# Performance work log

Measured on AMD Instinct MI355X. Metric: run time of the kernel, lower is better.

## Reference

```python
import jax, jax.numpy as jnp
import numpy as np

B, DIM, EMBDIM = 32, 512, 512
MEMSIZE, MEMSEQ = 32, 64
VOCAB = 50257


def setup_inputs() -> dict:
    key = jax.random.key(0)
    ks = jax.random.split(key, 10)
    inp = {
        'enc': jax.random.normal(ks[0], (B, DIM), jnp.float32),
        'encsumm': jax.random.normal(ks[1], (B, DIM), jnp.float32),
        'embsumm': jax.random.normal(ks[2], (B, EMBDIM), jnp.float32),
        'memencs': jax.random.normal(ks[3], (B, MEMSIZE, MEMSEQ, DIM), jnp.float32),
        'memencsumm': jax.random.normal(ks[4], (B, MEMSIZE, MEMSEQ, DIM), jnp.float32),
        'memembsumm': jax.random.normal(ks[5], (B, MEMSIZE, MEMSEQ, EMBDIM), jnp.float32),
        'memmask': jnp.ones((B, MEMSIZE, MEMSEQ), jnp.float32),
        'memids': jax.random.randint(ks[6], (B, MEMSIZE, MEMSEQ), 0, VOCAB, jnp.int64 if jax.config.jax_enable_x64 else jnp.int32),
        'W_out': jax.random.normal(ks[7], (VOCAB, 2 * DIM), jnp.float32) * 0.02,
        'b_out': jnp.zeros((VOCAB,), jnp.float32),
        'W_mix': jax.random.normal(ks[8], (2, 2 * DIM), jnp.float32) * 0.02,
        'b_mix': jnp.zeros((2,), jnp.float32),
        'unktok_mask': jnp.ones((VOCAB,), jnp.float32),  # no unktoks
    }
    return inp


def reference(enc, encsumm, embsumm, memencs, memencsumm, memembsumm, memmask,
              memids, W_out, b_out, W_mix, b_mix, unktok_mask):
    # copy branch: attention over flattened memory, scatter-add into vocab
    query = jnp.concatenate([embsumm, jnp.zeros_like(encsumm), enc], axis=-1)        # (B, 2*dim+embdim)
    keys = jnp.concatenate([memembsumm, jnp.zeros_like(memencsumm), memencs], axis=-1)  # (B, M, Z, 2*dim+embdim)
    w = jnp.einsum('bd,bmzd->bmz', query, keys) + jnp.log(memmask)
    b = w.shape[0]
    w = w.reshape(b, -1)                                    # (B, M*Z)
    alphas = jax.nn.softmax(w, axis=-1)
    mem_flat = memencs.reshape(b, -1, memencs.shape[-1])    # (B, M*Z, dim)
    mem_enc_summ = jnp.einsum('bm,bmd->bd', alphas, mem_flat)
    toks = memids.reshape(b, -1)                            # (B, M*Z)
    rows = jnp.arange(b)[:, None]
    vocsize = W_out.shape[0]
    probs_mem = jnp.zeros((b, vocsize), alphas.dtype).at[rows, toks].add(alphas)
    # generation branch
    h = jnp.concatenate([encsumm, enc], axis=-1)            # (B, 2*dim)
    logits_gen = h @ W_out.T + b_out + jnp.log(unktok_mask)[None, :]
    probs_gen = jax.nn.softmax(logits_gen, axis=-1)
    # mixer combine
    mix = jax.nn.softmax(h @ W_mix.T + b_mix, axis=-1)      # (B, 2)
    probs = mix[:, 0:1] * probs_gen + mix[:, 1:2] * probs_mem
    # original stack/gather trick: selects probs where nonzero, zeros where zero -> identity
    probs = jnp.where(probs != 0, probs, jnp.zeros_like(probs))
    return probs, mem_enc_summ
```

## Files before the change

kernel.cpp:

```cpp
#include <hip/hip_runtime.h>
#include <hip/hip_bf16.h>

#define NB   32
#define DIMK 512
#define MM   32
#define ZZ   64
#define MZV  2048
#define VOC  50257
#define NK4  1571

typedef __attribute__((ext_vector_type(8))) short  short8;
typedef __attribute__((ext_vector_type(4))) float  f32x4;
typedef __attribute__((ext_vector_type(8))) unsigned short ushort8;

#define WS_W      0
#define WS_PVEC   (WS_W + NB*MZV)
#define WS_LSTAT  (WS_PVEC + NB*MM*DIMK)
#define WS_GSTATW (WS_LSTAT + NB*MM*2)
#define WS_MIX    (WS_GSTATW + NB*2)
#define WS_GPART  (WS_MIX + NB*2)
#define WS_H      (WS_GPART + NB*32*2)

__device__ __forceinline__ ushort8 cvt8(float4 a, float4 b) {
    union { ushort8 u; __hip_bfloat162 h[4]; } r;
    r.h[0] = __float22bfloat162_rn(make_float2(a.x, a.y));
    r.h[1] = __float22bfloat162_rn(make_float2(a.z, a.w));
    r.h[2] = __float22bfloat162_rn(make_float2(b.x, b.y));
    r.h[3] = __float22bfloat162_rn(make_float2(b.z, b.w));
    return r.u;
}

typedef const __attribute__((address_space(1))) void* gas_t;
typedef __attribute__((address_space(3))) void*       las_t;
__device__ __forceinline__ void gload16(const void* g, void* l) {
    __builtin_amdgcn_global_load_lds((gas_t)g, (las_t)l, 16, 0, 0);
}

__global__ void k0_stageh(const float* __restrict__ encsumm, const float* __restrict__ enc,
                          float* __restrict__ ws)
{
    int b = blockIdx.x;
    int c = threadIdx.x * 4;
    const float* src = (c < DIMK) ? (encsumm + b*DIMK + c) : (enc + b*DIMK + (c - DIMK));
    float4 v = *(const float4*)src;
    union { ushort4 u; __hip_bfloat162 h[2]; } o;
    o.h[0] = __float22bfloat162_rn(make_float2(v.x, v.y));
    o.h[1] = __float22bfloat162_rn(make_float2(v.z, v.w));
    *(ushort4*)((unsigned short*)(ws + WS_H) + b*1024 + c) = o.u;
}

__global__ __launch_bounds__(256, 4) void k14_fused(
    const float* __restrict__ enc, const float* __restrict__ embsumm,
    const float* __restrict__ memencs, const float* __restrict__ memembsumm,
    const float* __restrict__ memmask,
    const unsigned short* __restrict__ hbf,
    const float* __restrict__ W_out, const float* __restrict__ b_out,
    const float* __restrict__ unk, float* __restrict__ out,
    float* __restrict__ ws)
{
    __shared__ __align__(16) union {
        struct { float sacc[4][DIMK]; float sst[4][2]; } s1;
        struct { float w[2][2048]; unsigned short a[2][2048]; } s4;
    } smem;

    int bid = blockIdx.x;
    int tid = threadIdx.x, wid = tid >> 6, lane = tid & 63;
    bool isK1; int sub;
    if (bid < 2048) { isK1 = ((bid & 1) == 0); sub = bid >> 1; }
    else            { isK1 = false;            sub = bid - 1024; }

    if (isK1) {
        int b = sub >> 5, m = sub & 31;
        int c0 = lane * 4, c1 = c0 + 256;
        const float* encb = enc + b * DIMK;
        const float* embb = embsumm + b * DIMK;
        float4 qe0 = *(const float4*)(encb + c0);
        float4 qe1 = *(const float4*)(encb + c1);
        float4 qm0 = *(const float4*)(embb + c0);
        float4 qm1 = *(const float4*)(embb + c1);
        const float* meb = memencs    + (long)(b*MM + m) * ZZ * DIMK;
        const float* mmb = memembsumm + (long)(b*MM + m) * ZZ * DIMK;
        const float* mkb = memmask    + (long)(b*MM + m) * ZZ;
        float* w_ws = ws + WS_W + b*MZV + m*ZZ;

        float lmax = -3.0e38f, lsum = 0.f;
        float4 a0 = make_float4(0.f,0.f,0.f,0.f), a1 = make_float4(0.f,0.f,0.f,0.f);

        for (int z = wid; z < ZZ; z += 4) {
            const float* mer = meb + z*DIMK;
            const float* mmr = mmb + z*DIMK;
            float4 e0 = *(const float4*)(mer + c0);
            float4 e1 = *(const float4*)(mer + c1);
            float4 s0 = *(const float4*)(mmr + c0);
            float4 s1 = *(const float4*)(mmr + c1);
            float d = e0.x*qe0.x + e0.y*qe0.y + e0.z*qe0.z + e0.w*qe0.w
                    + e1.x*qe1.x + e1.y*qe1.y + e1.z*qe1.z + e1.w*qe1.w
                    + s0.x*qm0.x + s0.y*qm0.y + s0.z*qm0.z + s0.w*qm0.w
                    + s1.x*qm1.x + s1.y*qm1.y + s1.z*qm1.z + s1.w*qm1.w;
            #pragma unroll
            for (int off = 32; off; off >>= 1) d += __shfl_xor(d, off);
            d += logf(mkb[z]);
            if (lane == 0) w_ws[z] = d;
            float nm = fmaxf(lmax, d);
            float sc = __expf(lmax - nm);
            float e  = __expf(d - nm);
            lsum = lsum * sc + e;
            a0.x = a0.x*sc + e*e0.x; a0.y = a0.y*sc + e*e0.y;
            a0.z = a0.z*sc + e*e0.z; a0.w = a0.w*sc + e*e0.w;
            a1.x = a1.x*sc + e*e1.x; a1.y = a1.y*sc + e*e1.y;
            a1.z = a1.z*sc + e*e1.z; a1.w = a1.w*sc + e*e1.w;
            lmax = nm;
        }

        *(float4*)&smem.s1.sacc[wid][c0] = a0;
        *(float4*)&smem.s1.sacc[wid][c1] = a1;
        if (lane == 0) { smem.s1.sst[wid][0] = lmax; smem.s1.sst[wid][1] = lsum; }
        __syncthreads();
        float bm = fmaxf(fmaxf(smem.s1.sst[0][0], smem.s1.sst[1][0]),
                         fmaxf(smem.s1.sst[2][0], smem.s1.sst[3][0]));
        float sc0 = __expf(smem.s1.sst[0][0]-bm), sc1 = __expf(smem.s1.sst[1][0]-bm);
        float sc2 = __expf(smem.s1.sst[2][0]-bm), sc3 = __expf(smem.s1.sst[3][0]-bm);
        float bs = smem.s1.sst[0][1]*sc0 + smem.s1.sst[1][1]*sc1
                 + smem.s1.sst[2][1]*sc2 + smem.s1.sst[3][1]*sc3;
        int d0 = tid * 2;
        float2 v0 = *(float2*)&smem.s1.sacc[0][d0];
        float2 v1 = *(float2*)&smem.s1.sacc[1][d0];
        float2 v2 = *(float2*)&smem.s1.sacc[2][d0];
        float2 v3 = *(float2*)&smem.s1.sacc[3][d0];
        float p0 = v0.x*sc0 + v1.x*sc1 + v2.x*sc2 + v3.x*sc3;
        float p1 = v0.y*sc0 + v1.y*sc1 + v2.y*sc2 + v3.y*sc3;
        float* pv = ws + WS_PVEC + (long)(b*MM+m)*DIMK + d0;
        pv[0] = p0; pv[1] = p1;
        if (tid == 0) { float* ls = ws + WS_LSTAT + (b*MM+m)*2; ls[0] = bm; ls[1] = bs; }
    } else {
        int wv = wid >> 1, wb = wid & 1;
        int vt = sub * 32;

        int idx0 = (wid*2 + 0)*64 + lane;
        int idx1 = (wid*2 + 1)*64 + lane;
        int wr0 = idx0 >> 4, wq0 = idx0 & 15;
        int wr1 = idx1 >> 4, wq1 = idx1 & 15;
        const float* wsrc0 = W_out + (long)min(vt + wr0, VOC-1)*1024 + ((wq0 ^ (wr0 & 7))*4);
        const float* wsrc1 = W_out + (long)min(vt + wr1, VOC-1)*1024 + ((wq1 ^ (wr1 & 7))*4);
        int aidx = wid*64 + lane;
        int ar = aidx >> 3, ag = aidx & 7;
        const unsigned short* asrc = hbf + ar*1024 + ((ag ^ (ar & 7))*8);

#define ISSUE(c, buf) do {                                            \
            gload16(wsrc0 + (c)*64, &smem.s4.w[buf][idx0*4]);         \
            gload16(wsrc1 + (c)*64, &smem.s4.w[buf][idx1*4]);         \
            gload16(asrc  + (c)*64, &smem.s4.a[buf][aidx*8]); } while (0)

        int lg = lane >> 4, ln = lane & 15;
        int vrow = wv*16 + ln;
        int ab   = wb*16 + ln;
        f32x4 acc = {0.f, 0.f, 0.f, 0.f};

        ISSUE(0, 0);
        ISSUE(1, 1);
        __syncthreads();

        for (int c = 0; c < 16; ++c) {
            int buf = c & 1;
            #pragma unroll
            for (int s = 0; s < 2; ++s) {
                int q = s*8 + lg*2;
                float4 b0 = *(const float4*)&smem.s4.w[buf][vrow*64 + ((q    ) ^ (vrow & 7))*4];
                float4 b1 = *(const float4*)&smem.s4.w[buf][vrow*64 + ((q + 1) ^ (vrow & 7))*4];
                int g = s*4 + lg;
                short8 afrag = *(const short8*)&smem.s4.a[buf][ab*64 + ((g ^ (ab & 7)))*8];
                ushort8 bu = cvt8(b0, b1);
                short8 bfrag = *(short8*)&bu;
                acc = __builtin_amdgcn_mfma_f32_16x16x32_bf16(afrag, bfrag, acc, 0, 0, 0);
            }
            __syncthreads();
            if (c + 2 < 16) ISSUE(c + 2, buf);
        }
#undef ISSUE

        int v = vt + vrow;
        if (v < VOC) {
            float bias = b_out[v] + logf(unk[v]);
            #pragma unroll
            for (int rr = 0; rr < 4; ++rr) {
                int m = wb*16 + lg*4 + rr;
                out[(long)m*VOC + v] = acc[rr] + bias;
            }
        }
    }
}

__global__ __launch_bounds__(256) void k2_comb(
    const float* __restrict__ encsumm, const float* __restrict__ enc,
    const float* __restrict__ W_mix, const float* __restrict__ b_mix,
    float* __restrict__ out, float* __restrict__ ws)
{
    int b = blockIdx.x, tid = threadIdx.x;
    const float* ls = ws + WS_LSTAT + b*MM*2;
    float gm = -3.0e38f;
    #pragma unroll
    for (int m = 0; m < MM; m++) gm = fmaxf(gm, ls[m*2]);
    float gs = 0.f;
    #pragma unroll
    for (int m = 0; m < MM; m++) gs += ls[m*2+1] * __expf(ls[m*2] - gm);
    if (tid == 0) { ws[WS_GSTATW + b*2] = gm; ws[WS_GSTATW + b*2 + 1] = gs; }
    float inv = 1.0f / gs;
    int d0 = tid * 2;
    float p0 = 0.f, p1 = 0.f;
    for (int m = 0; m < MM; m++) {
        float sc = __expf(ls[m*2] - gm);
        const float* pv = ws + WS_PVEC + (long)(b*MM+m)*DIMK + d0;
        p0 += pv[0]*sc; p1 += pv[1]*sc;
    }
    out[(long)NB*VOC + b*DIMK + d0]     = p0 * inv;
    out[(long)NB*VOC + b*DIMK + d0 + 1] = p1 * inv;

    if (tid < 64) {
        int l = tid;
        float m0 = 0.f, m1 = 0.f;
        #pragma unroll
        for (int p = 0; p < 4; p++) {
            int cc = l*4 + p*256;
            float4 h4 = (cc < 512) ? *(const float4*)(encsumm + b*DIMK + cc)
                                   : *(const float4*)(enc + b*DIMK + cc - 512);
            float4 w0 = *(const float4*)(W_mix + cc);
            float4 w1 = *(const float4*)(W_mix + 1024 + cc);
            m0 += h4.x*w0.x + h4.y*w0.y + h4.z*w0.z + h4.w*w0.w;
            m1 += h4.x*w1.x + h4.y*w1.y + h4.z*w1.z + h4.w*w1.w;
        }
        #pragma unroll
        for (int off = 32; off; off >>= 1) { m0 += __shfl_xor(m0, off); m1 += __shfl_xor(m1, off); }
        if (l == 0) {
            m0 += b_mix[0]; m1 += b_mix[1];
            float mx = fmaxf(m0, m1);
            float e0 = __expf(m0-mx), e1 = __expf(m1-mx);
            float s = e0 + e1;
            ws[WS_MIX + b*2] = e0/s; ws[WS_MIX + b*2 + 1] = e1/s;
        }
    }
}

__global__ __launch_bounds__(256) void k5_gstat(const float* __restrict__ logits, float* __restrict__ ws)
{
    int chunk = blockIdx.x, b = blockIdx.y, tid = threadIdx.x;
    const int CH = (VOC + 31) / 32;
    int v0 = chunk * CH;
    int v1 = min(VOC, v0 + CH);
    float m = -3.0e38f, s = 0.f;
    for (int v = v0 + tid; v < v1; v += 256) {
        float x = logits[(long)b*VOC + v];
        float nm = fmaxf(m, x);
        s = s*__expf(m - nm) + __expf(x - nm);
        m = nm;
    }
    #pragma unroll
    for (int off = 32; off; off >>= 1) {
        float om = __shfl_xor(m, off), os = __shfl_xor(s, off);
        float nm = fmaxf(m, om);
        s = s*__expf(m - nm) + os*__expf(om - nm);
        m = nm;
    }
    __shared__ float sm[4], ssum[4];
    int wid = tid >> 6, lane = tid & 63;
    if (lane == 0) { sm[wid] = m; ssum[wid] = s; }
    __syncthreads();
    if (tid == 0) {
        float gm = fmaxf(fmaxf(sm[0], sm[1]), fmaxf(sm[2], sm[3]));
        float gs = ssum[0]*__expf(sm[0]-gm) + ssum[1]*__expf(sm[1]-gm)
                 + ssum[2]*__expf(sm[2]-gm) + ssum[3]*__expf(sm[3]-gm);
        ws[WS_GPART + (b*32 + chunk)*2]     = gm;
        ws[WS_GPART + (b*32 + chunk)*2 + 1] = gs;
    }
}

__global__ __launch_bounds__(256) void k6_final(float* __restrict__ probs, const float* __restrict__ ws)
{
    int v = blockIdx.x*256 + threadIdx.x;
    int b = blockIdx.y;
    float gm = -3.0e38f;
    #pragma unroll
    for (int i = 0; i < 32; ++i) gm = fmaxf(gm, ws[WS_GPART + (b*32+i)*2]);
    float gs = 0.f;
    #pragma unroll
    for (int i = 0; i < 32; ++i)
        gs += ws[WS_GPART + (b*32+i)*2 + 1] * __expf(ws[WS_GPART + (b*32+i)*2] - gm);
    if (v >= VOC) return;
    float mix0 = ws[WS_MIX + b*2];
    long idx = (long)b*VOC + v;
    probs[idx] = mix0 * __expf(probs[idx] - gm) / gs;
}

__global__ __launch_bounds__(256) void k7_scatter(const int* __restrict__ memids,
                                                  const float* __restrict__ ws,
                                                  float* __restrict__ probs)
{
    int idx = blockIdx.x*256 + threadIdx.x;
    int b = idx >> 11, mz = idx & 2047;
    float gm = ws[WS_GSTATW + b*2], gs = ws[WS_GSTATW + b*2 + 1];
    float mix1 = ws[WS_MIX + b*2 + 1];
    float alpha = __expf(ws[WS_W + b*MZV + mz] - gm) / gs;
    int tok = memids[b*MZV + mz];
    atomicAdd(&probs[(long)b*VOC + tok], mix1 * alpha);
}

extern "C" void kernel_launch(void* const* d_in, const int* in_sizes, int n_in,
                              void* d_out, int out_size, void* d_ws, size_t ws_size,
                              hipStream_t stream)
{
    const float* enc        = (const float*)d_in[0];
    const float* encsumm    = (const float*)d_in[1];
    const float* embsumm    = (const float*)d_in[2];
    const float* memencs    = (const float*)d_in[3];
    const float* memembsumm = (const float*)d_in[5];
    const float* memmask    = (const float*)d_in[6];
    const int*   memids     = (const int*)d_in[7];
    const float* W_out      = (const float*)d_in[8];
    const float* b_out      = (const float*)d_in[9];
    const float* W_mix      = (const float*)d_in[10];
    const float* b_mix      = (const float*)d_in[11];
    const float* unk        = (const float*)d_in[12];
    float* out = (float*)d_out;
    float* ws  = (float*)d_ws;

    hipLaunchKernelGGL(k0_stageh, dim3(NB), dim3(256), 0, stream, encsumm, enc, ws);
    hipLaunchKernelGGL(k14_fused, dim3(1024 + NK4), dim3(256), 0, stream,
                       enc, embsumm, memencs, memembsumm, memmask,
                       (const unsigned short*)(ws + WS_H), W_out, b_out, unk, out, ws);
    hipLaunchKernelGGL(k2_comb, dim3(NB), dim3(256), 0, stream,
                       encsumm, enc, W_mix, b_mix, out, ws);
    hipLaunchKernelGGL(k5_gstat, dim3(32, NB), dim3(256), 0, stream, out, ws);
    hipLaunchKernelGGL(k6_final, dim3((VOC + 255)/256, NB), dim3(256), 0, stream, out, ws);
    hipLaunchKernelGGL(k7_scatter, dim3(NB*MZV/256), dim3(256), 0, stream, memids, ws, out);
}
```

Baseline: 137.1 us.

## Fold h bf16 staging into GEMM loop and merge comb/gstat kernels

Result: faster. 129.4 us (-5.7%).

```diff
diff --git a/kernel.cpp b/kernel.cpp
--- a/kernel.cpp
+++ b/kernel.cpp
@@ -19,7 +19,6 @@
 #define WS_GSTATW (WS_LSTAT + NB*MM*2)
 #define WS_MIX    (WS_GSTATW + NB*2)
 #define WS_GPART  (WS_MIX + NB*2)
-#define WS_H      (WS_GPART + NB*32*2)
 
 __device__ __forceinline__ ushort8 cvt8(float4 a, float4 b) {
     union { ushort8 u; __hip_bfloat162 h[4]; } r;
@@ -36,24 +35,11 @@
     __builtin_amdgcn_global_load_lds((gas_t)g, (las_t)l, 16, 0, 0);
 }
 
-__global__ void k0_stageh(const float* __restrict__ encsumm, const float* __restrict__ enc,
-                          float* __restrict__ ws)
-{
-    int b = blockIdx.x;
-    int c = threadIdx.x * 4;
-    const float* src = (c < DIMK) ? (encsumm + b*DIMK + c) : (enc + b*DIMK + (c - DIMK));
-    float4 v = *(const float4*)src;
-    union { ushort4 u; __hip_bfloat162 h[2]; } o;
-    o.h[0] = __float22bfloat162_rn(make_float2(v.x, v.y));
-    o.h[1] = __float22bfloat162_rn(make_float2(v.z, v.w));
-    *(ushort4*)((unsigned short*)(ws + WS_H) + b*1024 + c) = o.u;
-}
-
-__global__ __launch_bounds__(256, 4) void k14_fused(
+__global__ __launch_bounds__(256, 6) void k14_fused(
     const float* __restrict__ enc, const float* __restrict__ embsumm,
+    const float* __restrict__ encsumm,
     const float* __restrict__ memencs, const float* __restrict__ memembsumm,
     const float* __restrict__ memmask,
-    const unsigned short* __restrict__ hbf,
     const float* __restrict__ W_out, const float* __restrict__ b_out,
     const float* __restrict__ unk, float* __restrict__ out,
     float* __restrict__ ws)
@@ -142,22 +128,29 @@
         int wr1 = idx1 >> 4, wq1 = idx1 & 15;
         const float* wsrc0 = W_out + (long)min(vt + wr0, VOC-1)*1024 + ((wq0 ^ (wr0 & 7))*4);
         const float* wsrc1 = W_out + (long)min(vt + wr1, VOC-1)*1024 + ((wq1 ^ (wr1 & 7))*4);
-        int aidx = wid*64 + lane;
-        int ar = aidx >> 3, ag = aidx & 7;
-        const unsigned short* asrc = hbf + ar*1024 + ((ag ^ (ar & 7))*8);
-
-#define ISSUE(c, buf) do {                                            \
+        int ar = tid >> 3, ag = tid & 7;
+        const float* hs0 = encsumm + ar*DIMK + ag*8;
+        const float* hs1 = enc     + ar*DIMK + ag*8;
+        int awpos = ar*64 + ((ag ^ (ar & 7))*8);
+
+#define ISSUE_W(c, buf) do {                                          \
             gload16(wsrc0 + (c)*64, &smem.s4.w[buf][idx0*4]);         \
-            gload16(wsrc1 + (c)*64, &smem.s4.w[buf][idx1*4]);         \
-            gload16(asrc  + (c)*64, &smem.s4.a[buf][aidx*8]); } while (0)
+            gload16(wsrc1 + (c)*64, &smem.s4.w[buf][idx1*4]); } while (0)
+#define LOADA(c) do { const float* hp = ((c) < 8 ? hs0 + (c)*64 : hs1 + ((c)-8)*64); \
+            af0 = *(const float4*)(hp); af1 = *(const float4*)(hp + 4); } while (0)
+#define WRITEA(buf) do { *(ushort8*)&smem.s4.a[buf][awpos] = cvt8(af0, af1); } while (0)
 
         int lg = lane >> 4, ln = lane & 15;
         int vrow = wv*16 + ln;
         int ab   = wb*16 + ln;
         f32x4 acc = {0.f, 0.f, 0.f, 0.f};
-
-        ISSUE(0, 0);
-        ISSUE(1, 1);
+        float4 af0, af1;
+
+        LOADA(0); WRITEA(0);
+        LOADA(1); WRITEA(1);
+        LOADA(2);
+        ISSUE_W(0, 0);
+        ISSUE_W(1, 1);
         __syncthreads();
 
         for (int c = 0; c < 16; ++c) {
@@ -174,9 +167,15 @@
                 acc = __builtin_amdgcn_mfma_f32_16x16x32_bf16(afrag, bfrag, acc, 0, 0, 0);
             }
             __syncthreads();
-            if (c + 2 < 16) ISSUE(c + 2, buf);
-        }
-#undef ISSUE
+            if (c + 2 < 16) {
+                WRITEA(buf);
+                ISSUE_W(c + 2, buf);
+                if (c + 3 < 16) LOADA(c + 3);
+            }
+        }
+#undef ISSUE_W
+#undef LOADA
+#undef WRITEA
 
         int v = vt + vrow;
         if (v < VOC) {
@@ -190,86 +189,88 @@
     }
 }
 
-__global__ __launch_bounds__(256) void k2_comb(
+__global__ __launch_bounds__(256) void k2k5(
     const float* __restrict__ encsumm, const float* __restrict__ enc,
     const float* __restrict__ W_mix, const float* __restrict__ b_mix,
     float* __restrict__ out, float* __restrict__ ws)
 {
-    int b = blockIdx.x, tid = threadIdx.x;
-    const float* ls = ws + WS_LSTAT + b*MM*2;
-    float gm = -3.0e38f;
-    #pragma unroll
-    for (int m = 0; m < MM; m++) gm = fmaxf(gm, ls[m*2]);
-    float gs = 0.f;
-    #pragma unroll
-    for (int m = 0; m < MM; m++) gs += ls[m*2+1] * __expf(ls[m*2] - gm);
-    if (tid == 0) { ws[WS_GSTATW + b*2] = gm; ws[WS_GSTATW + b*2 + 1] = gs; }
-    float inv = 1.0f / gs;
-    int d0 = tid * 2;
-    float p0 = 0.f, p1 = 0.f;
-    for (int m = 0; m < MM; m++) {
-        float sc = __expf(ls[m*2] - gm);
-        const float* pv = ws + WS_PVEC + (long)(b*MM+m)*DIMK + d0;
-        p0 += pv[0]*sc; p1 += pv[1]*sc;
-    }
-    out[(long)NB*VOC + b*DIMK + d0]     = p0 * inv;
-    out[(long)NB*VOC + b*DIMK + d0 + 1] = p1 * inv;
-
-    if (tid < 64) {
-        int l = tid;
-        float m0 = 0.f, m1 = 0.f;
+    int bid = blockIdx.x, tid = threadIdx.x;
+    if (bid < 32) {
+        int b = bid;
+        const float* ls = ws + WS_LSTAT + b*MM*2;
+        float gm = -3.0e38f;
         #pragma unroll
-        for (int p = 0; p < 4; p++) {
-            int cc = l*4 + p*256;
-            float4 h4 = (cc < 512) ? *(const float4*)(encsumm + b*DIMK + cc)
-                                   : *(const float4*)(enc + b*DIMK + cc - 512);
-            float4 w0 = *(const float4*)(W_mix + cc);
-            float4 w1 = *(const float4*)(W_mix + 1024 + cc);
-            m0 += h4.x*w0.x + h4.y*w0.y + h4.z*w0.z + h4.w*w0.w;
-            m1 += h4.x*w1.x + h4.y*w1.y + h4.z*w1.z + h4.w*w1.w;
-        }
+        for (int m = 0; m < MM; m++) gm = fmaxf(gm, ls[m*2]);
+        float gs = 0.f;
         #pragma unroll
-        for (int off = 32; off; off >>= 1) { m0 += __shfl_xor(m0, off); m1 += __shfl_xor(m1, off); }
-        if (l == 0) {
-            m0 += b_mix[0]; m1 += b_mix[1];
-            float mx = fmaxf(m0, m1);
-            float e0 = __expf(m0-mx), e1 = __expf(m1-mx);
-            float s = e0 + e1;
-            ws[WS_MIX + b*2] = e0/s; ws[WS_MIX + b*2 + 1] = e1/s;
-        }
-    }
-}
-
-__global__ __launch_bounds__(256) void k5_gstat(const float* __restrict__ logits, float* __restrict__ ws)
-{
-    int chunk = blockIdx.x, b = blockIdx.y, tid = threadIdx.x;
-    const int CH = (VOC + 31) / 32;
-    int v0 = chunk * CH;
-    int v1 = min(VOC, v0 + CH);
-    float m = -3.0e38f, s = 0.f;
-    for (int v = v0 + tid; v < v1; v += 256) {
-        float x = logits[(long)b*VOC + v];
-        float nm = fmaxf(m, x);
-        s = s*__expf(m - nm) + __expf(x - nm);
-        m = nm;
-    }
-    #pragma unroll
-    for (int off = 32; off; off >>= 1) {
-        float om = __shfl_xor(m, off), os = __shfl_xor(s, off);
-        float nm = fmaxf(m, om);
-        s = s*__expf(m - nm) + os*__expf(om - nm);
-        m = nm;
-    }
-    __shared__ float sm[4], ssum[4];
-    int wid = tid >> 6, lane = tid & 63;
-    if (lane == 0) { sm[wid] = m; ssum[wid] = s; }
-    __syncthreads();
-    if (tid == 0) {
-        float gm = fmaxf(fmaxf(sm[0], sm[1]), fmaxf(sm[2], sm[3]));
-        float gs = ssum[0]*__expf(sm[0]-gm) + ssum[1]*__expf(sm[1]-gm)
-                 + ssum[2]*__expf(sm[2]-gm) + ssum[3]*__expf(sm[3]-gm);
-        ws[WS_GPART + (b*32 + chunk)*2]     = gm;
-        ws[WS_GPART + (b*32 + chunk)*2 + 1] = gs;
+        for (int m = 0; m < MM; m++) gs += ls[m*2+1] * __expf(ls[m*2] - gm);
+        if (tid == 0) { ws[WS_GSTATW + b*2] = gm; ws[WS_GSTATW + b*2 + 1] = gs; }
+        float inv = 1.0f / gs;
+        int d0 = tid * 2;
+        float p0 = 0.f, p1 = 0.f;
+        for (int m = 0; m < MM; m++) {
+            float sc = __expf(ls[m*2] - gm);
+            const float* pv = ws + WS_PVEC + (long)(b*MM+m)*DIMK + d0;
+            p0 += pv[0]*sc; p1 += pv[1]*sc;
+        }
+        out[(long)NB*VOC + b*DIMK + d0]     = p0 * inv;
+        out[(long)NB*VOC + b*DIMK + d0 + 1] = p1 * inv;
+
+        if (tid < 64) {
+            int l = tid;
+            float m0 = 0.f, m1 = 0.f;
+            #pragma unroll
+            for (int p = 0; p < 4; p++) {
+                int cc = l*4 + p*256;
+                float4 h4 = (cc < 512) ? *(const float4*)(encsumm + b*DIMK + cc)
+                                       : *(const float4*)(enc + b*DIMK + cc - 512);
+                float4 w0 = *(const float4*)(W_mix + cc);
+                float4 w1 = *(const float4*)(W_mix + 1024 + cc);
+                m0 += h4.x*w0.x + h4.y*w0.y + h4.z*w0.z + h4.w*w0.w;
+                m1 += h4.x*w1.x + h4.y*w1.y + h4.z*w1.z + h4.w*w1.w;
+            }
+            #pragma unroll
+            for (int off = 32; off; off >>= 1) { m0 += __shfl_xor(m0, off); m1 += __shfl_xor(m1, off); }
+            if (l == 0) {
+                m0 += b_mix[0]; m1 += b_mix[1];
+                float mx = fmaxf(m0, m1);
+                float e0 = __expf(m0-mx), e1 = __expf(m1-mx);
+                float s = e0 + e1;
+                ws[WS_MIX + b*2] = e0/s; ws[WS_MIX + b*2 + 1] = e1/s;
+            }
+        }
+    } else {
+        int sub = bid - 32;
+        int chunk = sub & 31, b = sub >> 5;
+        const float* logits = out;
+        const int CH = (VOC + 31) / 32;
+        int v0 = chunk * CH;
+        int v1 = min(VOC, v0 + CH);
+        float m = -3.0e38f, s = 0.f;
+        for (int v = v0 + tid; v < v1; v += 256) {
+            float x = logits[(long)b*VOC + v];
+            float nm = fmaxf(m, x);
+            s = s*__expf(m - nm) + __expf(x - nm);
+            m = nm;
+        }
+        #pragma unroll
+        for (int off = 32; off; off >>= 1) {
+            float om = __shfl_xor(m, off), os = __shfl_xor(s, off);
+            float nm = fmaxf(m, om);
+            s = s*__expf(m - nm) + os*__expf(om - nm);
+            m = nm;
+        }
+        __shared__ float sm[4], ssum[4];
+        int wid = tid >> 6, lane = tid & 63;
+        if (lane == 0) { sm[wid] = m; ssum[wid] = s; }
+        __syncthreads();
+        if (tid == 0) {
+            float gm = fmaxf(fmaxf(sm[0], sm[1]), fmaxf(sm[2], sm[3]));
+            float gs = ssum[0]*__expf(sm[0]-gm) + ssum[1]*__expf(sm[1]-gm)
+                     + ssum[2]*__expf(sm[2]-gm) + ssum[3]*__expf(sm[3]-gm);
+            ws[WS_GPART + (b*32 + chunk)*2]     = gm;
+            ws[WS_GPART + (b*32 + chunk)*2 + 1] = gs;
+        }
     }
 }
 
@@ -322,13 +323,11 @@
     float* out = (float*)d_out;
     float* ws  = (float*)d_ws;
 
-    hipLaunchKernelGGL(k0_stageh, dim3(NB), dim3(256), 0, stream, encsumm, enc, ws);
     hipLaunchKernelGGL(k14_fused, dim3(1024 + NK4), dim3(256), 0, stream,
-                       enc, embsumm, memencs, memembsumm, memmask,
-                       (const unsigned short*)(ws + WS_H), W_out, b_out, unk, out, ws);
-    hipLaunchKernelGGL(k2_comb, dim3(NB), dim3(256), 0, stream,
+                       enc, embsumm, encsumm, memencs, memembsumm, memmask,
+                       W_out, b_out, unk, out, ws);
+    hipLaunchKernelGGL(k2k5, dim3(32 + 1024), dim3(256), 0, stream,
                        encsumm, enc, W_mix, b_mix, out, ws);
-    hipLaunchKernelGGL(k5_gstat, dim3(32, NB), dim3(256), 0, stream, out, ws);
     hipLaunchKernelGGL(k6_final, dim3((VOC + 255)/256, NB), dim3(256), 0, stream, out, ws);
     hipLaunchKernelGGL(k7_scatter, dim3(NB*MZV/256), dim3(256), 0, stream, memids, ws, out);
 }
```
